# Kernel tuning notes

Hardware: AMD Instinct MI355X
Metric: run time of the kernel (lower is better)

Reference implementation:

```python
import jax, jax.numpy as jnp
import numpy as np
import math

B, T, E, H = 2, 2048, 1024, 16
HD = E // H
EPS = 1e-5


def rope(x):
    # x: [B,H,T,HD]. Faithful to source: cos/sin built from cat(freqs,freqs),
    # rotation uses interleaved pairing of even/odd channels.
    d = x.shape[-1]
    t = x.shape[-2]
    inv_freq = 1.0 / (10000.0 ** (jnp.arange(0, d, 2, dtype=jnp.float32) / d))
    freqs = jnp.arange(t, dtype=jnp.float32)[:, None] * inv_freq[None, :]  # [T, d/2]
    emb = jnp.concatenate([freqs, freqs], axis=-1)  # [T, d]
    cos = jnp.cos(emb)[None, None]  # [1,1,T,d]
    sin = jnp.sin(emb)[None, None]
    x1 = x[..., ::2]
    x2 = x[..., 1::2]
    x_rot = jnp.stack([-x2, x1], axis=-1).reshape(x.shape)
    return x * cos + x_rot * sin


def group_norm(y, w, b):
    # y: [B,T,E] -> normalize per (batch, head-group) over (HD, T) like torch GroupNorm on (B,E,T)
    yt = jnp.transpose(y, (0, 2, 1))  # [B,E,T]
    g = yt.reshape(B, H, HD * T)
    mu = jnp.mean(g, axis=-1, keepdims=True)
    var = jnp.var(g, axis=-1, keepdims=True)
    g = (g - mu) * jax.lax.rsqrt(var + EPS)
    yt = g.reshape(B, E, T) * w[None, :, None] + b[None, :, None]
    return jnp.transpose(yt, (0, 2, 1))


def setup_inputs() -> dict:
    key = jax.random.key(0)
    ks = jax.random.split(key, 13)
    s = 1.0 / math.sqrt(E)
    d = {"x": jax.random.normal(ks[0], (B, T, E), jnp.float32)}
    for i, n in enumerate(["q", "k", "v", "g", "o"]):
        d[f"W{n}"] = jax.random.uniform(ks[1 + 2 * i], (E, E), jnp.float32, -s, s)
        d[f"b{n}"] = jax.random.uniform(ks[2 + 2 * i], (E,), jnp.float32, -s, s)
    d["gn_w"] = jnp.ones((E,), jnp.float32)
    d["gn_b"] = jnp.zeros((E,), jnp.float32)
    return d


def reference(x, Wq, bq, Wk, bk, Wv, bv, Wg, bg, Wo, bo, gn_w, gn_b):
    scale = math.sqrt(HD)
    def proj(W, b):
        return (x @ W.T + b).reshape(B, T, H, HD).transpose(0, 2, 1, 3)  # [B,H,T,HD]
    Q = rope(proj(Wq, bq))
    K = rope(proj(Wk, bk))
    V = proj(Wv, bv)

    # decay mask exactly as in source: m=col idx, n=row idx; mask = (m>=n)*gamma^(m-n)
    gamma = 1.0 - 2.0 ** (-5.0 - jnp.arange(H, dtype=jnp.float32))  # [H]
    m = jnp.arange(T)[None, :]
    n = jnp.arange(T)[:, None]
    diff = (m - n).astype(jnp.float32)  # [T,T]
    mask = jnp.where(m >= n, gamma[:, None, None] ** diff[None], 0.0)  # [H,T,T]

    scores = jnp.einsum("bhid,bhjd->bhij", Q, K) / scale
    scores = scores * mask[None]
    out = jnp.einsum("bhij,bhjd->bhid", scores, V)  # [B,H,T,HD]
    out = out.transpose(0, 2, 1, 3).reshape(B, T, E)
    out = group_norm(out, gn_w, gn_b)
    gate = jax.nn.silu(x @ Wg.T + bg)
    return (gate * out) @ Wo.T + bo
```

## Files before the change

### kernel.cpp

```cpp
#include <hip/hip_runtime.h>
#include <math.h>

typedef unsigned short u16;
typedef unsigned int u32;
typedef __attribute__((ext_vector_type(8))) short short8;
typedef __attribute__((ext_vector_type(4))) float f32x4;

#define BB 2
#define TT 2048
#define EE 1024
#define HH 16
#define HDD 64
#define NC 32
#define CS 64

__device__ __forceinline__ float bf2f(u16 u){ union{unsigned i; float f;} v; v.i=((unsigned)u)<<16; return v.f; }
__device__ __forceinline__ u16 f2bf(float f){ union{float f; unsigned i;} v; v.f=f; return (u16)((v.i + 0x7fffu + ((v.i>>16)&1u))>>16); }

__device__ __forceinline__ void gload16(const void* g, void* l){
    __builtin_amdgcn_global_load_lds((const __attribute__((address_space(1))) void*)g,
                                     (__attribute__((address_space(3))) void*)l, 16, 0, 0);
}

__global__ __launch_bounds__(256)
void cvt_swz(const float* __restrict__ s0, const float* __restrict__ s1,
             const float* __restrict__ s2, const float* __restrict__ s3,
             const float* __restrict__ s4, const float* __restrict__ s5,
             u16* __restrict__ d0, u16* __restrict__ d1, u16* __restrict__ d2,
             u16* __restrict__ d3, u16* __restrict__ d4, u16* __restrict__ d5)
{
    const float* S; u16* D; int nch;
    switch (blockIdx.z) {
        case 0: S=s0; D=d0; nch=4096*128; break;
        case 1: S=s1; D=d1; nch=1024*128; break;
        case 2: S=s2; D=d2; nch=1024*128; break;
        case 3: S=s3; D=d3; nch=1024*128; break;
        case 4: S=s4; D=d4; nch=1024*128; break;
        default:S=s5; D=d5; nch=1024*128; break;
    }
    int ci = blockIdx.x*256 + threadIdx.x;
    if (ci >= nch) return;
    int r = ci >> 7, c = ci & 127;
    int pc = (c & ~3) | ((c & 3) ^ ((r >> 1) & 3));
    const float4* sp = (const float4*)(S + (size_t)r*EE + c*8);
    float4 f0 = sp[0], f1 = sp[1];
    short8 ov; u16* o = (u16*)&ov;
    o[0]=f2bf(f0.x); o[1]=f2bf(f0.y); o[2]=f2bf(f0.z); o[3]=f2bf(f0.w);
    o[4]=f2bf(f1.x); o[5]=f2bf(f1.y); o[6]=f2bf(f1.z); o[7]=f2bf(f1.w);
    *(short8*)(D + (size_t)r*EE + pc*8) = ov;
}

__global__ __launch_bounds__(256)
void trig_tab(float* __restrict__ ctab, float* __restrict__ stab)
{
    int idx = blockIdx.x*256 + threadIdx.x;
    int t = idx >> 5, f = idx & 31;
    float ang = (float)t * exp2f(-(float)f * (13.287712379549449f/32.f));
    ctab[idx] = cosf(ang);
    stab[idx] = sinf(ang);
}

__global__ __launch_bounds__(512)
void gemm_qkvg(const u16* __restrict__ A,
               const u16* __restrict__ W0, const u16* __restrict__ W1,
               const u16* __restrict__ W2, const u16* __restrict__ W3,
               const float* __restrict__ b0, const float* __restrict__ b1,
               const float* __restrict__ b2, const float* __restrict__ b3,
               u16* __restrict__ C0, u16* __restrict__ C1,
               u16* __restrict__ C2, u16* __restrict__ C3)
{
    __shared__ u16 SA[3][256*32];
    __shared__ u16 SB[3][256*32];
    const u16* W; const float* bias; u16* C; int swz;
    switch (blockIdx.z) {
        case 0: W=W0; bias=b0; C=C0; swz=1; break;
        case 1: W=W1; bias=b1; C=C1; swz=1; break;
        case 2: W=W2; bias=b2; C=C2; swz=0; break;
        default:W=W3; bias=b3; C=C3; swz=0; break;
    }
    const int bm = blockIdx.y*256, bn = blockIdx.x*256;
    const int tid = threadIdx.x;
    const int lane = tid & 63, g = lane >> 4, rl = lane & 15;
    const int w = tid >> 6, wr = w >> 2, wc = w & 3;

    auto STAGE = [&](int slot, int kt) {
        int k0 = kt*32;
        #pragma unroll
        for (int r2 = 0; r2 < 2; ++r2) {
            int cc = tid + 512*r2;
            int row = cc >> 2, ch = cc & 3;
            gload16(A + (size_t)(bm + row)*EE + k0 + ch*8, &SA[slot][cc*8]);
        }
        #pragma unroll
        for (int r2 = 0; r2 < 2; ++r2) {
            int cc = tid + 512*r2;
            int row = cc >> 2, ch = cc & 3;
            gload16(W + (size_t)(bn + row)*EE + k0 + ch*8, &SB[slot][cc*8]);
        }
    };

    f32x4 acc[8][4] = {};
    STAGE(0, 0); STAGE(1, 1);
    for (int t = 0; t < 32; ++t) {
        if (t < 31) asm volatile("s_waitcnt vmcnt(4)" ::: "memory");
        else        asm volatile("s_waitcnt vmcnt(0)" ::: "memory");
        __builtin_amdgcn_s_barrier();
        int cur = t % 3;
        if (t + 2 < 32) STAGE((t+2) % 3, t+2);
        const u16* SAc = SA[cur]; const u16* SBc = SB[cur];
        short8 a[8], b[4];
        #pragma unroll
        for (int i = 0; i < 8; ++i) {
            int m = wr*128 + i*16 + rl;
            a[i] = *(const short8*)&SAc[m*32 + ((g ^ ((m>>1)&3)) << 3)];
        }
        #pragma unroll
        for (int j = 0; j < 4; ++j) {
            int n = wc*64 + j*16 + rl;
            b[j] = *(const short8*)&SBc[n*32 + ((g ^ ((n>>1)&3)) << 3)];
        }
        #pragma unroll
        for (int i = 0; i < 8; ++i)
            #pragma unroll
            for (int j = 0; j < 4; ++j)
                acc[i][j] = __builtin_amdgcn_mfma_f32_16x16x32_bf16(a[i], b[j], acc[i][j], 0, 0, 0);
    }
    float bj[4];
    #pragma unroll
    for (int j = 0; j < 4; ++j) bj[j] = bias[bn + wc*64 + j*16 + rl];
    #pragma unroll
    for (int i = 0; i < 8; ++i)
      #pragma unroll
      for (int rr = 0; rr < 4; ++rr) {
        int m = bm + wr*128 + i*16 + g*4 + rr;
        #pragma unroll
        for (int j = 0; j < 4; ++j) {
            int n = bn + wc*64 + j*16 + rl;
            float v = acc[i][j][rr] + bj[j];
            int col = swz ? ((n & ~63) | ((((n>>3)&7) ^ (m&7)) << 3) | (n & 7)) : n;
            C[(size_t)m*EE + col] = f2bf(v);
        }
      }
}

__global__ __launch_bounds__(256)
void gemm_out(const u16* __restrict__ A, const u16* __restrict__ W,
              const float* __restrict__ bias, float* __restrict__ C)
{
    __shared__ u16 SA[3][128*32];
    __shared__ u16 SB[3][128*32];
    const int bm = blockIdx.y*128, bn = blockIdx.x*128;
    const int tid = threadIdx.x;
    const int lane = tid & 63, g = lane >> 4, rl = lane & 15;
    const int w = tid >> 6, wr = w >> 1, wc = w & 1;

    auto STAGE = [&](int slot, int kt) {
        int k0 = kt*32;
        #pragma unroll
        for (int r2 = 0; r2 < 2; ++r2) {
            int cc = tid + 256*r2;
            int row = cc >> 2, ch = cc & 3;
            gload16(A + (size_t)(bm + row)*EE + k0 + ch*8, &SA[slot][cc*8]);
        }
        #pragma unroll
        for (int r2 = 0; r2 < 2; ++r2) {
            int cc = tid + 256*r2;
            int row = cc >> 2, ch = cc & 3;
            gload16(W + (size_t)(bn + row)*EE + k0 + ch*8, &SB[slot][cc*8]);
        }
    };

    f32x4 acc[4][4] = {};
    STAGE(0, 0); STAGE(1, 1);
    for (int t = 0; t < 32; ++t) {
        if (t < 31) asm volatile("s_waitcnt vmcnt(4)" ::: "memory");
        else        asm volatile("s_waitcnt vmcnt(0)" ::: "memory");
        __builtin_amdgcn_s_barrier();
        int cur = t % 3;
        if (t + 2 < 32) STAGE((t+2) % 3, t+2);
        const u16* SAc = SA[cur]; const u16* SBc = SB[cur];
        short8 a[4], b[4];
        #pragma unroll
        for (int i = 0; i < 4; ++i) {
            int m = wr*64 + i*16 + rl;
            a[i] = *(const short8*)&SAc[m*32 + ((g ^ ((m>>1)&3)) << 3)];
            int n = wc*64 + i*16 + rl;
            b[i] = *(const short8*)&SBc[n*32 + ((g ^ ((n>>1)&3)) << 3)];
        }
        #pragma unroll
        for (int i = 0; i < 4; ++i)
            #pragma unroll
            for (int j = 0; j < 4; ++j)
                acc[i][j] = __builtin_amdgcn_mfma_f32_16x16x32_bf16(a[i], b[j], acc[i][j], 0, 0, 0);
    }
    float bj[4];
    #pragma unroll
    for (int j = 0; j < 4; ++j) bj[j] = bias[bn + wc*64 + j*16 + rl];
    #pragma unroll
    for (int i = 0; i < 4; ++i)
      #pragma unroll
      for (int rr = 0; rr < 4; ++rr) {
        int m = bm + wr*64 + i*16 + g*4 + rr;
        #pragma unroll
        for (int j = 0; j < 4; ++j) {
            int n = bn + wc*64 + j*16 + rl;
            C[(size_t)m*EE + n] = acc[i][j][rr] + bj[j];
        }
      }
}

__global__ __launch_bounds__(256)
void rope_swz(u16* __restrict__ Q, u16* __restrict__ K,
              const float* __restrict__ ctab, const float* __restrict__ stab)
{
    u16* X = blockIdx.z ? K : Q;
    int ci = blockIdx.x*256 + threadIdx.x;
    int row = ci >> 7;
    int t = row & (TT-1);
    int c = ci & 127, h = c >> 3, p = c & 7;
    int d0 = (p ^ (t & 7)) << 3;
    u16* ptr = X + (size_t)row*EE + h*HDD + p*8;
    short8 xv = *(short8*)ptr;
    u16* xu = (u16*)&xv;
    const float* cr = ctab + t*32;
    const float* sr = stab + t*32;
    short8 ov; u16* o = (u16*)&ov;
    #pragma unroll
    for (int q = 0; q < 4; ++q) {
        int j0 = d0 + 2*q;
        float xe = bf2f(xu[2*q]), xo = bf2f(xu[2*q+1]);
        float c0 = cr[j0 & 31],     s0 = sr[j0 & 31];
        float c1 = cr[(j0+1) & 31], s1 = sr[(j0+1) & 31];
        o[2*q]   = f2bf(xe*c0 - xo*s0);
        o[2*q+1] = f2bf(xo*c1 + xe*s1);
    }
    *(short8*)ptr = ov;
}

__global__ __launch_bounds__(256)
void transV(const u16* __restrict__ V, u16* __restrict__ VT)
{
    __shared__ u16 ts[64*64];
    int t0 = blockIdx.x * 64, h = blockIdx.y, b = blockIdx.z;
    int tid = threadIdx.x;
    #pragma unroll
    for (int rr = 0; rr < 2; ++rr) {
        int cc = tid + rr*256;
        int r = cc >> 3, c = cc & 7;
        short8 v = *(const short8*)(V + (size_t)(b*TT + t0 + r)*EE + h*HDD + c*8);
        *(short8*)&ts[r*64 + ((c ^ (r & 7)) << 3)] = v;
    }
    __syncthreads();
    #pragma unroll
    for (int rr = 0; rr < 2; ++rr) {
        int oc = tid + rr*256;
        int d = oc & 63, tp = oc >> 6;
        short8 ov; u16* o = (u16*)&ov;
        #pragma unroll
        for (int e = 0; e < 8; ++e) {
            int t = tp*8 + e;
            o[e] = ts[t*64 + (((d>>3) ^ (t & 7)) << 3) + (d & 7)];
        }
        int ptp = tp ^ (d & 7);
        *(short8*)(VT + ((size_t)((b*HH + h)*HDD + d))*TT + t0 + ptp*8) = ov;
    }
}

__global__ __launch_bounds__(256)
void transK(const u16* __restrict__ K, u16* __restrict__ KT)
{
    __shared__ u16 ts[64*64];
    int t0 = blockIdx.x * 64, h = blockIdx.y, b = blockIdx.z;
    int tid = threadIdx.x;
    const float l2g = log2f(1.f - exp2f(-5.f - (float)h));
    #pragma unroll
    for (int rr = 0; rr < 2; ++rr) {
        int cc = tid + rr*256;
        int r = cc >> 3, c = cc & 7;
        short8 v = *(const short8*)(K + (size_t)(b*TT + t0 + r)*EE + h*HDD + c*8);
        *(short8*)&ts[r*64 + (c << 3)] = v;
    }
    __syncthreads();
    #pragma unroll
    for (int rr = 0; rr < 2; ++rr) {
        int oc = tid + rr*256;
        int d = oc & 63, tp = oc >> 6;
        short8 ov; u16* o = (u16*)&ov;
        #pragma unroll
        for (int e = 0; e < 8; ++e) {
            int t = tp*8 + e;
            float val = bf2f(ts[t*64 + (((d>>3) ^ (t & 7)) << 3) + (d & 7)]);
            o[e] = f2bf(val * exp2f(l2g * (float)t));
        }
        int ptp = tp ^ (d & 7);
        *(short8*)(KT + ((size_t)((b*HH + h)*HDD + d))*TT + t0 + ptp*8) = ov;
    }
}

__global__ __launch_bounds__(256)
void chunk_state(const u16* __restrict__ KT, const u16* __restrict__ VT,
                 float* __restrict__ Tb)
{
    __shared__ u16 Ks[64*64], Vs[64*64];
    const int tid = threadIdx.x, w = tid >> 6, lane = tid & 63;
    const int g = lane >> 4, rl = lane & 15;
    const int c = blockIdx.x, h = blockIdx.y, b = blockIdx.z;
    const int t0 = c*64;
    const size_t rowb = (size_t)((b*HH + h)*HDD);
    {
        int cc = tid, r = cc >> 3, ch = cc & 7;
        gload16(KT + (rowb + r)*TT + t0 + ch*8, &Ks[cc*8]);
        gload16(VT + (rowb + r)*TT + t0 + ch*8, &Vs[cc*8]);
        cc = tid + 256; r = cc >> 3; ch = cc & 7;
        gload16(KT + (rowb + r)*TT + t0 + ch*8, &Ks[cc*8]);
        gload16(VT + (rowb + r)*TT + t0 + ch*8, &Vs[cc*8]);
    }
    __syncthreads();
    int d2r = w*16 + rl;
    short8 af0 = *(const short8*)&Vs[d2r*64 + ((g ^ (d2r & 7)) << 3)];
    short8 af1 = *(const short8*)&Vs[d2r*64 + (((4+g) ^ (d2r & 7)) << 3)];
    f32x4 acc[4] = {};
    #pragma unroll
    for (int j = 0; j < 4; ++j) {
        int d1r = j*16 + rl;
        short8 b0 = *(const short8*)&Ks[d1r*64 + ((g ^ (d1r & 7)) << 3)];
        short8 b1 = *(const short8*)&Ks[d1r*64 + (((4+g) ^ (d1r & 7)) << 3)];
        acc[j] = __builtin_amdgcn_mfma_f32_16x16x32_bf16(af0, b0, acc[j], 0, 0, 0);
        acc[j] = __builtin_amdgcn_mfma_f32_16x16x32_bf16(af1, b1, acc[j], 0, 0, 0);
    }
    float* tb = Tb + ((size_t)((b*HH + h)*NC + c))*4096;
    #pragma unroll
    for (int j = 0; j < 4; ++j)
        #pragma unroll
        for (int rr = 0; rr < 4; ++rr)
            tb[(w*16 + g*4 + rr)*64 + j*16 + rl] = acc[j][rr];
}

__global__ __launch_bounds__(256)
void suffix_scan(const float* __restrict__ Tb, u16* __restrict__ Zb)
{
    __shared__ float lds[NC*512];
    const int q = blockIdx.x & 7;
    const int h = (blockIdx.x >> 3) & 15;
    const int b = blockIdx.x >> 7;
    const float l2g = log2f(1.f - exp2f(-5.f - (float)h));
    const float g64 = exp2f(l2g * 64.f);
    const float* tb = Tb + ((size_t)((b*HH + h)*NC))*4096 + q*512;
    u16* zb = Zb + ((size_t)((b*HH + h)*NC))*4096;
    const int tid = threadIdx.x;
    #pragma unroll
    for (int k = 0; k < 16; ++k) {
        int i4 = tid + k*256;
        int c = i4 >> 7, r = i4 & 127;
        *(float4*)&lds[c*512 + r*4] = *(const float4*)(tb + (size_t)c*4096 + r*4);
    }
    __syncthreads();
    int e0 = tid*2;
    int d2l = e0 >> 6, d1 = e0 & 63;
    int d2 = q*8 + d2l;
    int pos = d2*64 + (((d1>>3) ^ (d2 & 7)) << 3) + (d1 & 7);
    *(u32*)(zb + (size_t)31*4096 + pos) = 0u;
    float z0 = 0.f, z1 = 0.f;
    for (int c = 30; c >= 0; --c) {
        z0 = lds[(c+1)*512 + e0]     + g64*z0;
        z1 = lds[(c+1)*512 + e0 + 1] + g64*z1;
        u32 pk = (u32)f2bf(z0) | ((u32)f2bf(z1) << 16);
        *(u32*)(zb + (size_t)c*4096 + pos) = pk;
    }
}

__global__ __launch_bounds__(256)
void ret_out(const u16* __restrict__ Q, const u16* __restrict__ K,
             const u16* __restrict__ VT, const u16* __restrict__ Zb,
             float* __restrict__ R)
{
    __shared__ u16 Qs[64*64], Ks[64*64], Vs[64*64], Zs[64*64], Ss[64*64];
    const int tid = threadIdx.x, w = tid >> 6, lane = tid & 63;
    const int g = lane >> 4, rl = lane & 15;
    const int c = blockIdx.x, h = blockIdx.y, b = blockIdx.z;
    const int m0 = c*64;
    const float l2g = log2f(1.f - exp2f(-5.f - (float)h));
    const size_t vrow = (size_t)((b*HH + h)*HDD);
    const u16* zc = Zb + ((size_t)((b*HH + h)*NC + c))*4096;
    {
        int cc = tid, r = cc >> 3, ch = cc & 7;
        gload16(Q  + (size_t)(b*TT + m0 + r)*EE + h*HDD + ch*8, &Qs[cc*8]);
        gload16(K  + (size_t)(b*TT + m0 + r)*EE + h*HDD + ch*8, &Ks[cc*8]);
        gload16(VT + (vrow + r)*TT + m0 + ch*8, &Vs[cc*8]);
        gload16(zc + cc*8, &Zs[cc*8]);
        cc = tid + 256; r = cc >> 3; ch = cc & 7;
        gload16(Q  + (size_t)(b*TT + m0 + r)*EE + h*HDD + ch*8, &Qs[cc*8]);
        gload16(K  + (size_t)(b*TT + m0 + r)*EE + h*HDD + ch*8, &Ks[cc*8]);
        gload16(VT + (vrow + r)*TT + m0 + ch*8, &Vs[cc*8]);
        gload16(zc + cc*8, &Zs[cc*8]);
    }
    __syncthreads();
    const int mr = w*16 + rl;
    short8 qf[2];
    qf[0] = *(const short8*)&Qs[mr*64 + ((g ^ (rl & 7)) << 3)];
    qf[1] = *(const short8*)&Qs[mr*64 + (((4+g) ^ (rl & 7)) << 3)];
    f32x4 sacc[4] = {};
    #pragma unroll
    for (int j = 0; j < 4; ++j) {
        int n = j*16 + rl;
        short8 k0 = *(const short8*)&Ks[n*64 + ((g ^ (n & 7)) << 3)];
        short8 k1 = *(const short8*)&Ks[n*64 + (((4+g) ^ (n & 7)) << 3)];
        sacc[j] = __builtin_amdgcn_mfma_f32_16x16x32_bf16(qf[0], k0, sacc[j], 0, 0, 0);
        sacc[j] = __builtin_amdgcn_mfma_f32_16x16x32_bf16(qf[1], k1, sacc[j], 0, 0, 0);
    }
    float pn[4], pmv[4];
    #pragma unroll
    for (int j = 0; j < 4; ++j) pn[j] = exp2f(l2g * (float)(j*16 + rl));
    #pragma unroll
    for (int rr = 0; rr < 4; ++rr) pmv[rr] = exp2f(-l2g * (float)(w*16 + g*4 + rr));
    #pragma unroll
    for (int j = 0; j < 4; ++j) {
        int nl = j*16 + rl;
        #pragma unroll
        for (int rr = 0; rr < 4; ++rr) {
            int ml = w*16 + g*4 + rr;
            float wgt = (nl >= ml) ? 0.125f * pn[j] * pmv[rr] : 0.f;
            Ss[ml*64 + (((nl>>3) ^ (ml & 7)) << 3) + (nl & 7)] = f2bf(sacc[j][rr] * wgt);
        }
    }
    asm volatile("s_waitcnt lgkmcnt(0)" ::: "memory");
    f32x4 oacc[4] = {}, zacc[4] = {};
    #pragma unroll
    for (int s = 0; s < 2; ++s) {
        short8 sf = *(const short8*)&Ss[mr*64 + (((s*4 + g) ^ (rl & 7)) << 3)];
        #pragma unroll
        for (int j = 0; j < 4; ++j) {
            int d = j*16 + rl;
            short8 vf = *(const short8*)&Vs[d*64 + (((s*4 + g) ^ (d & 7)) << 3)];
            oacc[j] = __builtin_amdgcn_mfma_f32_16x16x32_bf16(sf, vf, oacc[j], 0, 0, 0);
            short8 zf = *(const short8*)&Zs[d*64 + (((s*4 + g) ^ (d & 7)) << 3)];
            zacc[j] = __builtin_amdgcn_mfma_f32_16x16x32_bf16(qf[s], zf, zacc[j], 0, 0, 0);
        }
    }
    const float g64 = exp2f(l2g * 64.f);
    #pragma unroll
    for (int j = 0; j < 4; ++j)
        #pragma unroll
        for (int rr = 0; rr < 4; ++rr) {
            int m_g = m0 + w*16 + g*4 + rr;
            float rs = 0.125f * g64 * pmv[rr];
            R[(size_t)(b*TT + m_g)*EE + h*HDD + j*16 + rl] = oacc[j][rr] + rs*zacc[j][rr];
        }
}

__global__ __launch_bounds__(256)
void gn_partial(const float* __restrict__ R, float* __restrict__ part)
{
    int bid = blockIdx.x;
    int bh = bid >> 4, seg = bid & 15;
    int b = bh >> 4, h = bh & 15;
    const float* base = R + (size_t)(b*TT + seg*128)*EE + h*HDD;
    float s = 0.f, sq = 0.f;
    #pragma unroll
    for (int k = 0; k < 8; ++k) {
        int i4 = threadIdx.x + 256*k;
        int t = i4 >> 4, dq = i4 & 15;
        float4 v = *(const float4*)(base + (size_t)t*EE + dq*4);
        s  += v.x + v.y + v.z + v.w;
        sq += v.x*v.x + v.y*v.y + v.z*v.z + v.w*v.w;
    }
    #pragma unroll
    for (int off = 32; off; off >>= 1) { s += __shfl_down(s, off, 64); sq += __shfl_down(sq, off, 64); }
    __shared__ float ls[4], lq[4];
    int lane = threadIdx.x & 63, wv = threadIdx.x >> 6;
    if (lane == 0) { ls[wv] = s; lq[wv] = sq; }
    __syncthreads();
    if (threadIdx.x == 0) {
        part[2*bid]   = ls[0]+ls[1]+ls[2]+ls[3];
        part[2*bid+1] = lq[0]+lq[1]+lq[2]+lq[3];
    }
}

__global__ void gn_finalize(const float* __restrict__ part, float* __restrict__ stats)
{
    int bh = threadIdx.x;
    if (bh < 32) {
        float s = 0.f, sq = 0.f;
        #pragma unroll
        for (int k = 0; k < 16; ++k) { s += part[2*(bh*16+k)]; sq += part[2*(bh*16+k)+1]; }
        const float inv = 1.f / (float)(TT*HDD);
        float mu = s * inv;
        float var = sq * inv - mu*mu;
        stats[2*bh]   = mu;
        stats[2*bh+1] = rsqrtf(var + 1e-5f);
    }
}

__global__ __launch_bounds__(256)
void zgate(const u16* __restrict__ G, const float* __restrict__ R,
           const float* __restrict__ stats, const float* __restrict__ gw,
           const float* __restrict__ gb, u16* __restrict__ Z)
{
    int ci = blockIdx.x*256 + threadIdx.x;
    int row = ci >> 7;
    int c = ci & 127;
    int e0 = c*8;
    int b = row >> 11;
    int bh = b*HH + (e0 >> 6);
    float mu = stats[2*bh], rs = stats[2*bh+1];
    short8 gv = *(const short8*)(G + (size_t)row*EE + e0);
    const u16* gu = (const u16*)&gv;
    const float* rp = R + (size_t)row*EE + e0;
    float4 r0 = *(const float4*)rp, r1 = *(const float4*)(rp+4);
    float rr[8] = {r0.x,r0.y,r0.z,r0.w,r1.x,r1.y,r1.z,r1.w};
    short8 ov; u16* o = (u16*)&ov;
    #pragma unroll
    for (int q = 0; q < 8; ++q) {
        float gvf = bf2f(gu[q]);
        float gate = gvf / (1.f + __expf(-gvf));
        float nv = (rr[q] - mu)*rs*gw[e0+q] + gb[e0+q];
        o[q] = f2bf(gate*nv);
    }
    int pc = (c & ~3) | ((c & 3) ^ ((row >> 1) & 3));
    *(short8*)(Z + (size_t)row*EE + pc*8) = ov;
}

extern "C" void kernel_launch(void* const* d_in, const int* in_sizes, int n_in,
                              void* d_out, int out_size, void* d_ws, size_t ws_size,
                              hipStream_t stream)
{
    const float* x  = (const float*)d_in[0];
    const float* Wq = (const float*)d_in[1];
    const float* bq = (const float*)d_in[2];
    const float* Wk = (const float*)d_in[3];
    const float* bk = (const float*)d_in[4];
    const float* Wv = (const float*)d_in[5];
    const float* bv = (const float*)d_in[6];
    const float* Wg = (const float*)d_in[7];
    const float* bg = (const float*)d_in[8];
    const float* Wo = (const float*)d_in[9];
    const float* bo = (const float*)d_in[10];
    const float* gw = (const float*)d_in[11];
    const float* gb = (const float*)d_in[12];
    float* out = (float*)d_out;

    char* p = (char*)d_ws;
    u16* xb  = (u16*)p;              p += (size_t)8<<20;
    u16* Wqb = (u16*)p;              p += (size_t)2<<20;
    u16* Wkb = (u16*)p;              p += (size_t)2<<20;
    u16* Wvb = (u16*)p;              p += (size_t)2<<20;
    u16* Wgb = (u16*)p;              p += (size_t)2<<20;
    u16* Wob = (u16*)p;              p += (size_t)2<<20;
    u16* Qb  = (u16*)p;              p += (size_t)8<<20;
    u16* Kb  = (u16*)p;              p += (size_t)8<<20;
    u16* Vb  = (u16*)p;              p += (size_t)8<<20;
    u16* Gb  = (u16*)p;              p += (size_t)8<<20;
    u16* VTb = (u16*)p;              p += (size_t)8<<20;
    u16* KTb = (u16*)p;              p += (size_t)8<<20;
    float* TbRb  = (float*)p;        p += (size_t)16<<20;
    float* part  = (float*)p;        p += 4096;
    float* stats = (float*)p;        p += 256;
    float* ctab  = (float*)p;        p += (size_t)65536*4;
    float* stab  = (float*)p;        p += (size_t)65536*4;
    u16* Zbuf = xb;
    float* Tb = TbRb;
    float* Rb = TbRb;
    u16* ZGb = xb;

    cvt_swz<<<dim3(2048,1,6), 256, 0, stream>>>(x, Wq, Wk, Wv, Wg, Wo,
                                                xb, Wqb, Wkb, Wvb, Wgb, Wob);
    trig_tab<<<256, 256, 0, stream>>>(ctab, stab);
    gemm_qkvg<<<dim3(4,16,4), 512, 0, stream>>>(xb, Wqb, Wkb, Wvb, Wgb,
                                                bq, bk, bv, bg, Qb, Kb, Vb, Gb);
    rope_swz<<<dim3(2048,1,2), 256, 0, stream>>>(Qb, Kb, ctab, stab);
    transV<<<dim3(32,16,2), 256, 0, stream>>>(Vb, VTb);
    transK<<<dim3(32,16,2), 256, 0, stream>>>(Kb, KTb);
    chunk_state<<<dim3(32,16,2), 256, 0, stream>>>(KTb, VTb, Tb);
    suffix_scan<<<256, 256, 0, stream>>>(Tb, Zbuf);
    ret_out<<<dim3(32,16,2), 256, 0, stream>>>(Qb, Kb, VTb, Zbuf, Rb);
    gn_partial<<<512, 256, 0, stream>>>(Rb, part);
    gn_finalize<<<1, 64, 0, stream>>>(part, stats);
    zgate<<<2048, 256, 0, stream>>>(Gb, Rb, stats, gw, gb, ZGb);
    gemm_out<<<dim3(8,32,1), 256, 0, stream>>>(ZGb, Wob, bo, out);
}
```

Measured before the change: 230.9 us.

## Restructure QKVG GEMM pipeline and fuse small kernels and group-norm stats

The QKVG GEMM is rewritten with BK=64 double-buffered LDS, an XOR-8 swizzle, per-quadrant MFMA phases with barriers, and s_setprio to interleave loads with compute. The input conversion swizzle changes to match. Trig table generation is folded into the conversion launch, and the V and K transposes merge into one kernel. Group-norm statistics are now accumulated with atomics in ret_out's epilogue, which removes the gn_partial and gn_finalize passes over R. These changes cut launch count and one full read of R, at the cost of a more complex GEMM schedule and atomic float ordering nondeterminism.

```diff
diff --git a/kernel.cpp b/kernel.cpp
--- a/kernel.cpp
+++ b/kernel.cpp
@@ -27,21 +27,32 @@
              const float* __restrict__ s2, const float* __restrict__ s3,
              const float* __restrict__ s4, const float* __restrict__ s5,
              u16* __restrict__ d0, u16* __restrict__ d1, u16* __restrict__ d2,
-             u16* __restrict__ d3, u16* __restrict__ d4, u16* __restrict__ d5)
-{
-    const float* S; u16* D; int nch;
+             u16* __restrict__ d3, u16* __restrict__ d4, u16* __restrict__ d5,
+             float* __restrict__ ctab, float* __restrict__ stab)
+{
+    if (blockIdx.z == 6) {
+        if (blockIdx.x >= 256) return;
+        int idx = blockIdx.x*256 + threadIdx.x;
+        int t = idx >> 5, f = idx & 31;
+        float ang = (float)t * exp2f(-(float)f * (13.287712379549449f/32.f));
+        ctab[idx] = cosf(ang);
+        stab[idx] = sinf(ang);
+        return;
+    }
+    const float* S; u16* D; int nch; int oldswz = 0;
     switch (blockIdx.z) {
         case 0: S=s0; D=d0; nch=4096*128; break;
         case 1: S=s1; D=d1; nch=1024*128; break;
         case 2: S=s2; D=d2; nch=1024*128; break;
         case 3: S=s3; D=d3; nch=1024*128; break;
         case 4: S=s4; D=d4; nch=1024*128; break;
-        default:S=s5; D=d5; nch=1024*128; break;
+        default:S=s5; D=d5; nch=1024*128; oldswz=1; break;
     }
     int ci = blockIdx.x*256 + threadIdx.x;
     if (ci >= nch) return;
     int r = ci >> 7, c = ci & 127;
-    int pc = (c & ~3) | ((c & 3) ^ ((r >> 1) & 3));
+    int pc = oldswz ? ((c & ~3) | ((c & 3) ^ ((r >> 1) & 3)))
+                    : ((c & ~7) | ((c & 7) ^ (r & 7)));
     const float4* sp = (const float4*)(S + (size_t)r*EE + c*8);
     float4 f0 = sp[0], f1 = sp[1];
     short8 ov; u16* o = (u16*)&ov;
@@ -50,17 +61,7 @@
     *(short8*)(D + (size_t)r*EE + pc*8) = ov;
 }
 
-__global__ __launch_bounds__(256)
-void trig_tab(float* __restrict__ ctab, float* __restrict__ stab)
-{
-    int idx = blockIdx.x*256 + threadIdx.x;
-    int t = idx >> 5, f = idx & 31;
-    float ang = (float)t * exp2f(-(float)f * (13.287712379549449f/32.f));
-    ctab[idx] = cosf(ang);
-    stab[idx] = sinf(ang);
-}
-
-__global__ __launch_bounds__(512)
+__global__ __launch_bounds__(512, 2)
 void gemm_qkvg(const u16* __restrict__ A,
                const u16* __restrict__ W0, const u16* __restrict__ W1,
                const u16* __restrict__ W2, const u16* __restrict__ W3,
@@ -69,8 +70,8 @@
                u16* __restrict__ C0, u16* __restrict__ C1,
                u16* __restrict__ C2, u16* __restrict__ C3)
 {
-    __shared__ u16 SA[3][256*32];
-    __shared__ u16 SB[3][256*32];
+    __shared__ u16 AS[2][16384];
+    __shared__ u16 BS[2][16384];
     const u16* W; const float* bias; u16* C; int swz;
     switch (blockIdx.z) {
         case 0: W=W0; bias=b0; C=C0; swz=1; break;
@@ -83,48 +84,97 @@
     const int lane = tid & 63, g = lane >> 4, rl = lane & 15;
     const int w = tid >> 6, wr = w >> 2, wc = w & 3;
 
-    auto STAGE = [&](int slot, int kt) {
-        int k0 = kt*32;
+    auto stage_half = [&](int isB, int kt, int half){
+        const u16* src = isB ? W : A;
+        int bb = isB ? bn : bm;
+        u16* dst = (isB ? &BS[kt&1][0] : &AS[kt&1][0]) + half*8192;
         #pragma unroll
         for (int r2 = 0; r2 < 2; ++r2) {
             int cc = tid + 512*r2;
-            int row = cc >> 2, ch = cc & 3;
-            gload16(A + (size_t)(bm + row)*EE + k0 + ch*8, &SA[slot][cc*8]);
-        }
-        #pragma unroll
-        for (int r2 = 0; r2 < 2; ++r2) {
-            int cc = tid + 512*r2;
-            int row = cc >> 2, ch = cc & 3;
-            gload16(W + (size_t)(bn + row)*EE + k0 + ch*8, &SB[slot][cc*8]);
+            int hr = cc >> 3, pcc = cc & 7;
+            gload16(src + (size_t)(bb + half*128 + hr)*EE + kt*64 + pcc*8, dst + cc*8);
         }
     };
-
+    short8 a[8], bf0[4], bf1[4];
+    auto read_a = [&](int bi, int Mh){
+        const u16* base = &AS[bi][wr*8192];
+        #pragma unroll
+        for (int mb = 0; mb < 4; ++mb)
+          #pragma unroll
+          for (int kh = 0; kh < 2; ++kh) {
+            int hr = Mh*64 + mb*16 + rl;
+            a[mb*2+kh] = *(const short8*)&base[hr*64 + (((kh*4+g) ^ (hr&7)) << 3)];
+          }
+    };
+    auto read_b = [&](short8 (&bf)[4], int bi, int Nh){
+        #pragma unroll
+        for (int nb = 0; nb < 2; ++nb)
+          #pragma unroll
+          for (int kh = 0; kh < 2; ++kh) {
+            int nr = wc*64 + Nh*32 + nb*16 + rl;
+            int half = nr >> 7, hr = nr & 127;
+            bf[nb*2+kh] = *(const short8*)&BS[bi][half*8192 + hr*64 + (((kh*4+g) ^ (hr&7)) << 3)];
+          }
+    };
     f32x4 acc[8][4] = {};
-    STAGE(0, 0); STAGE(1, 1);
-    for (int t = 0; t < 32; ++t) {
-        if (t < 31) asm volatile("s_waitcnt vmcnt(4)" ::: "memory");
-        else        asm volatile("s_waitcnt vmcnt(0)" ::: "memory");
-        __builtin_amdgcn_s_barrier();
-        int cur = t % 3;
-        if (t + 2 < 32) STAGE((t+2) % 3, t+2);
-        const u16* SAc = SA[cur]; const u16* SBc = SB[cur];
-        short8 a[8], b[4];
-        #pragma unroll
-        for (int i = 0; i < 8; ++i) {
-            int m = wr*128 + i*16 + rl;
-            a[i] = *(const short8*)&SAc[m*32 + ((g ^ ((m>>1)&3)) << 3)];
-        }
-        #pragma unroll
-        for (int j = 0; j < 4; ++j) {
-            int n = wc*64 + j*16 + rl;
-            b[j] = *(const short8*)&SBc[n*32 + ((g ^ ((n>>1)&3)) << 3)];
-        }
-        #pragma unroll
-        for (int i = 0; i < 8; ++i)
+    auto mfma_q = [&](short8 (&bf)[4], int Mh, int Nh){
+        __builtin_amdgcn_s_setprio(1);
+        #pragma unroll
+        for (int mb = 0; mb < 4; ++mb)
+          #pragma unroll
+          for (int nb = 0; nb < 2; ++nb)
             #pragma unroll
-            for (int j = 0; j < 4; ++j)
-                acc[i][j] = __builtin_amdgcn_mfma_f32_16x16x32_bf16(a[i], b[j], acc[i][j], 0, 0, 0);
-    }
+            for (int kh = 0; kh < 2; ++kh)
+              acc[Mh*4+mb][Nh*2+nb] = __builtin_amdgcn_mfma_f32_16x16x32_bf16(
+                  a[mb*2+kh], bf[nb*2+kh], acc[Mh*4+mb][Nh*2+nb], 0, 0, 0);
+        __builtin_amdgcn_s_setprio(0);
+    };
+    #define BAR()    __builtin_amdgcn_s_barrier()
+    #define LGKM0()  { asm volatile("s_waitcnt lgkmcnt(0)" ::: "memory"); __builtin_amdgcn_sched_barrier(0); }
+    #define VM4()    asm volatile("s_waitcnt vmcnt(4)" ::: "memory")
+
+    stage_half(0,0,0); stage_half(0,0,1); stage_half(1,0,0); stage_half(1,0,1);
+    stage_half(1,1,0); stage_half(1,1,1);
+    VM4(); BAR();
+
+    for (int i = 0; i < 7; ++i) {
+        int k1 = 2*i+1, k2 = 2*i+2, k3 = 2*i+3;
+        read_a(0,0); read_b(bf0,0,0); stage_half(0,k1,0);
+        BAR(); LGKM0(); mfma_q(bf0,0,0); BAR();
+        read_b(bf1,0,1); stage_half(0,k1,1);
+        BAR(); LGKM0(); mfma_q(bf1,0,1); BAR();
+        read_a(0,1); stage_half(1,k2,0);
+        BAR(); LGKM0(); mfma_q(bf0,1,0); BAR();
+        stage_half(1,k2,1); VM4();
+        BAR(); mfma_q(bf1,1,1); BAR();
+        read_a(1,0); read_b(bf0,1,0); stage_half(0,k2,0);
+        BAR(); LGKM0(); mfma_q(bf0,0,0); BAR();
+        read_b(bf1,1,1); stage_half(0,k2,1);
+        BAR(); LGKM0(); mfma_q(bf1,0,1); BAR();
+        read_a(1,1); stage_half(1,k3,0);
+        BAR(); LGKM0(); mfma_q(bf0,1,0); BAR();
+        stage_half(1,k3,1); VM4();
+        BAR(); mfma_q(bf1,1,1); BAR();
+    }
+    read_a(0,0); read_b(bf0,0,0); stage_half(0,15,0);
+    BAR(); LGKM0(); mfma_q(bf0,0,0); BAR();
+    read_b(bf1,0,1); stage_half(0,15,1);
+    BAR(); LGKM0(); mfma_q(bf1,0,1); BAR();
+    read_a(0,1);
+    BAR(); LGKM0(); mfma_q(bf0,1,0); BAR();
+    asm volatile("s_waitcnt vmcnt(0)" ::: "memory");
+    BAR(); mfma_q(bf1,1,1); BAR();
+    read_a(1,0); read_b(bf0,1,0);
+    BAR(); LGKM0(); mfma_q(bf0,0,0); BAR();
+    read_b(bf1,1,1);
+    BAR(); LGKM0(); mfma_q(bf1,0,1); BAR();
+    read_a(1,1);
+    BAR(); LGKM0(); mfma_q(bf0,1,0); BAR();
+    mfma_q(bf1,1,1);
+    #undef BAR
+    #undef LGKM0
+    #undef VM4
+
     float bj[4];
     #pragma unroll
     for (int j = 0; j < 4; ++j) bj[j] = bias[bn + wc*64 + j*16 + rl];
@@ -238,17 +288,23 @@
 }
 
 __global__ __launch_bounds__(256)
-void transV(const u16* __restrict__ V, u16* __restrict__ VT)
+void transKV(const u16* __restrict__ V, const u16* __restrict__ K,
+             u16* __restrict__ VT, u16* __restrict__ KT)
 {
     __shared__ u16 ts[64*64];
-    int t0 = blockIdx.x * 64, h = blockIdx.y, b = blockIdx.z;
+    int t0 = blockIdx.x * 64, h = blockIdx.y;
+    int b = blockIdx.z & 1, kind = blockIdx.z >> 1;
+    const u16* src = kind ? K : V;
+    u16* dst = kind ? KT : VT;
     int tid = threadIdx.x;
+    const float l2g = log2f(1.f - exp2f(-5.f - (float)h));
     #pragma unroll
     for (int rr = 0; rr < 2; ++rr) {
         int cc = tid + rr*256;
         int r = cc >> 3, c = cc & 7;
-        short8 v = *(const short8*)(V + (size_t)(b*TT + t0 + r)*EE + h*HDD + c*8);
-        *(short8*)&ts[r*64 + ((c ^ (r & 7)) << 3)] = v;
+        short8 v = *(const short8*)(src + (size_t)(b*TT + t0 + r)*EE + h*HDD + c*8);
+        int sc = kind ? c : (c ^ (r & 7));
+        *(short8*)&ts[r*64 + (sc << 3)] = v;
     }
     __syncthreads();
     #pragma unroll
@@ -259,41 +315,11 @@
         #pragma unroll
         for (int e = 0; e < 8; ++e) {
             int t = tp*8 + e;
-            o[e] = ts[t*64 + (((d>>3) ^ (t & 7)) << 3) + (d & 7)];
+            u16 raw = ts[t*64 + (((d>>3) ^ (t & 7)) << 3) + (d & 7)];
+            o[e] = kind ? f2bf(bf2f(raw) * exp2f(l2g * (float)t)) : raw;
         }
         int ptp = tp ^ (d & 7);
-        *(short8*)(VT + ((size_t)((b*HH + h)*HDD + d))*TT + t0 + ptp*8) = ov;
-    }
-}
-
-__global__ __launch_bounds__(256)
-void transK(const u16* __restrict__ K, u16* __restrict__ KT)
-{
-    __shared__ u16 ts[64*64];
-    int t0 = blockIdx.x * 64, h = blockIdx.y, b = blockIdx.z;
-    int tid = threadIdx.x;
-    const float l2g = log2f(1.f - exp2f(-5.f - (float)h));
-    #pragma unroll
-    for (int rr = 0; rr < 2; ++rr) {
-        int cc = tid + rr*256;
-        int r = cc >> 3, c = cc & 7;
-        short8 v = *(const short8*)(K + (size_t)(b*TT + t0 + r)*EE + h*HDD + c*8);
-        *(short8*)&ts[r*64 + (c << 3)] = v;
-    }
-    __syncthreads();
-    #pragma unroll
-    for (int rr = 0; rr < 2; ++rr) {
-        int oc = tid + rr*256;
-        int d = oc & 63, tp = oc >> 6;
-        short8 ov; u16* o = (u16*)&ov;
-        #pragma unroll
-        for (int e = 0; e < 8; ++e) {
-            int t = tp*8 + e;
-            float val = bf2f(ts[t*64 + (((d>>3) ^ (t & 7)) << 3) + (d & 7)]);
-            o[e] = f2bf(val * exp2f(l2g * (float)t));
-        }
-        int ptp = tp ^ (d & 7);
-        *(short8*)(KT + ((size_t)((b*HH + h)*HDD + d))*TT + t0 + ptp*8) = ov;
+        *(short8*)(dst + ((size_t)((b*HH + h)*HDD + d))*TT + t0 + ptp*8) = ov;
     }
 }
 
@@ -372,9 +398,10 @@
 __global__ __launch_bounds__(256)
 void ret_out(const u16* __restrict__ Q, const u16* __restrict__ K,
              const u16* __restrict__ VT, const u16* __restrict__ Zb,
-             float* __restrict__ R)
+             float* __restrict__ R, float* __restrict__ part2)
 {
     __shared__ u16 Qs[64*64], Ks[64*64], Vs[64*64], Zs[64*64], Ss[64*64];
+    __shared__ float reds[4], redq[4];
     const int tid = threadIdx.x, w = tid >> 6, lane = tid & 63;
     const int g = lane >> 4, rl = lane & 15;
     const int c = blockIdx.x, h = blockIdx.y, b = blockIdx.z;
@@ -438,62 +465,31 @@
         }
     }
     const float g64 = exp2f(l2g * 64.f);
+    float s = 0.f, sq = 0.f;
     #pragma unroll
     for (int j = 0; j < 4; ++j)
         #pragma unroll
         for (int rr = 0; rr < 4; ++rr) {
             int m_g = m0 + w*16 + g*4 + rr;
             float rs = 0.125f * g64 * pmv[rr];
-            R[(size_t)(b*TT + m_g)*EE + h*HDD + j*16 + rl] = oacc[j][rr] + rs*zacc[j][rr];
-        }
-}
-
-__global__ __launch_bounds__(256)
-void gn_partial(const float* __restrict__ R, float* __restrict__ part)
-{
-    int bid = blockIdx.x;
-    int bh = bid >> 4, seg = bid & 15;
-    int b = bh >> 4, h = bh & 15;
-    const float* base = R + (size_t)(b*TT + seg*128)*EE + h*HDD;
-    float s = 0.f, sq = 0.f;
-    #pragma unroll
-    for (int k = 0; k < 8; ++k) {
-        int i4 = threadIdx.x + 256*k;
-        int t = i4 >> 4, dq = i4 & 15;
-        float4 v = *(const float4*)(base + (size_t)t*EE + dq*4);
-        s  += v.x + v.y + v.z + v.w;
-        sq += v.x*v.x + v.y*v.y + v.z*v.z + v.w*v.w;
-    }
+            float val = oacc[j][rr] + rs*zacc[j][rr];
+            R[(size_t)(b*TT + m_g)*EE + h*HDD + j*16 + rl] = val;
+            s += val; sq += val*val;
+        }
     #pragma unroll
     for (int off = 32; off; off >>= 1) { s += __shfl_down(s, off, 64); sq += __shfl_down(sq, off, 64); }
-    __shared__ float ls[4], lq[4];
-    int lane = threadIdx.x & 63, wv = threadIdx.x >> 6;
-    if (lane == 0) { ls[wv] = s; lq[wv] = sq; }
+    if (lane == 0) { reds[w] = s; redq[w] = sq; }
     __syncthreads();
-    if (threadIdx.x == 0) {
-        part[2*bid]   = ls[0]+ls[1]+ls[2]+ls[3];
-        part[2*bid+1] = lq[0]+lq[1]+lq[2]+lq[3];
-    }
-}
-
-__global__ void gn_finalize(const float* __restrict__ part, float* __restrict__ stats)
-{
-    int bh = threadIdx.x;
-    if (bh < 32) {
-        float s = 0.f, sq = 0.f;
-        #pragma unroll
-        for (int k = 0; k < 16; ++k) { s += part[2*(bh*16+k)]; sq += part[2*(bh*16+k)+1]; }
-        const float inv = 1.f / (float)(TT*HDD);
-        float mu = s * inv;
-        float var = sq * inv - mu*mu;
-        stats[2*bh]   = mu;
-        stats[2*bh+1] = rsqrtf(var + 1e-5f);
+    if (tid == 0) {
+        int bh = b*HH + h;
+        atomicAdd(&part2[2*bh],   reds[0]+reds[1]+reds[2]+reds[3]);
+        atomicAdd(&part2[2*bh+1], redq[0]+redq[1]+redq[2]+redq[3]);
     }
 }
 
 __global__ __launch_bounds__(256)
 void zgate(const u16* __restrict__ G, const float* __restrict__ R,
-           const float* __restrict__ stats, const float* __restrict__ gw,
+           const float* __restrict__ part2, const float* __restrict__ gw,
            const float* __restrict__ gb, u16* __restrict__ Z)
 {
     int ci = blockIdx.x*256 + threadIdx.x;
@@ -502,7 +498,10 @@
     int e0 = c*8;
     int b = row >> 11;
     int bh = b*HH + (e0 >> 6);
-    float mu = stats[2*bh], rs = stats[2*bh+1];
+    const float inv = 1.f / (float)(TT*HDD);
+    float mu = part2[2*bh] * inv;
+    float var = part2[2*bh+1] * inv - mu*mu;
+    float rs = rsqrtf(var + 1e-5f);
     short8 gv = *(const short8*)(G + (size_t)row*EE + e0);
     const u16* gu = (const u16*)&gv;
     const float* rp = R + (size_t)row*EE + e0;
@@ -553,8 +552,7 @@
     u16* VTb = (u16*)p;              p += (size_t)8<<20;
     u16* KTb = (u16*)p;              p += (size_t)8<<20;
     float* TbRb  = (float*)p;        p += (size_t)16<<20;
-    float* part  = (float*)p;        p += 4096;
-    float* stats = (float*)p;        p += 256;
+    float* part2 = (float*)p;        p += 4096;
     float* ctab  = (float*)p;        p += (size_t)65536*4;
     float* stab  = (float*)p;        p += (size_t)65536*4;
     u16* Zbuf = xb;
@@ -562,19 +560,17 @@
     float* Rb = TbRb;
     u16* ZGb = xb;
 
-    cvt_swz<<<dim3(2048,1,6), 256, 0, stream>>>(x, Wq, Wk, Wv, Wg, Wo,
-                                                xb, Wqb, Wkb, Wvb, Wgb, Wob);
-    trig_tab<<<256, 256, 0, stream>>>(ctab, stab);
+    hipMemsetAsync(part2, 0, 64*sizeof(float), stream);
+    cvt_swz<<<dim3(2048,1,7), 256, 0, stream>>>(x, Wq, Wk, Wv, Wg, Wo,
+                                                xb, Wqb, Wkb, Wvb, Wgb, Wob,
+                                                ctab, stab);
     gemm_qkvg<<<dim3(4,16,4), 512, 0, stream>>>(xb, Wqb, Wkb, Wvb, Wgb,
                                                 bq, bk, bv, bg, Qb, Kb, Vb, Gb);
     rope_swz<<<dim3(2048,1,2), 256, 0, stream>>>(Qb, Kb, ctab, stab);
-    transV<<<dim3(32,16,2), 256, 0, stream>>>(Vb, VTb);
-    transK<<<dim3(32,16,2), 256, 0, stream>>>(Kb, KTb);
+    transKV<<<dim3(32,16,4), 256, 0, stream>>>(Vb, Kb, VTb, KTb);
     chunk_state<<<dim3(32,16,2), 256, 0, stream>>>(KTb, VTb, Tb);
     suffix_scan<<<256, 256, 0, stream>>>(Tb, Zbuf);
-    ret_out<<<dim3(32,16,2), 256, 0, stream>>>(Qb, Kb, VTb, Zbuf, Rb);
-    gn_partial<<<512, 256, 0, stream>>>(Rb, part);
-    gn_finalize<<<1, 64, 0, stream>>>(part, stats);
-    zgate<<<2048, 256, 0, stream>>>(Gb, Rb, stats, gw, gb, ZGb);
+    ret_out<<<dim3(32,16,2), 256, 0, stream>>>(Qb, Kb, VTb, Zbuf, Rb, part2);
+    zgate<<<2048, 256, 0, stream>>>(Gb, Rb, part2, gw, gb, ZGb);
     gemm_out<<<dim3(8,32,1), 256, 0, stream>>>(ZGb, Wob, bo, out);
 }
```

Measured after the change: 223.6 us. 1.03x faster.
